# Performance work log

Measured on AMD Instinct MI355X. Metric: run time of the kernel, lower is better.

Reference implementation:

```python
import jax, jax.numpy as jnp
import numpy as np

NUM_HEADS = 16


def setup_inputs() -> dict:
    key = jax.random.key(0)
    ks = jax.random.split(key, 7)
    B, S, H = 4, 1024, 1024
    s = 0.02
    return {
        "x": jax.random.normal(ks[0], (B, S, H), dtype=jnp.float32),
        "Wq": jax.random.normal(ks[1], (H, H), dtype=jnp.float32) * s,
        "bq": jax.random.normal(ks[2], (H,), dtype=jnp.float32) * s,
        "Wk": jax.random.normal(ks[3], (H, H), dtype=jnp.float32) * s,
        "bk": jax.random.normal(ks[4], (H,), dtype=jnp.float32) * s,
        "Wv": jax.random.normal(ks[5], (H, H), dtype=jnp.float32) * s,
        "bv": jax.random.normal(ks[6], (H,), dtype=jnp.float32) * s,
    }


def _split_heads(y, num_heads):
    # rearrange 'b s (h c) -> h b s c'
    b, s, hid = y.shape
    c = hid // num_heads
    return y.reshape(b, s, num_heads, c).transpose(2, 0, 1, 3)


def reference(x, Wq, bq, Wk, bk, Wv, bv):
    h = NUM_HEADS
    head_size = x.shape[-1] // h
    # torch Linear: y = x @ W.T + b
    q = _split_heads(x @ Wq.T + bq, h)  # [h,b,s,c]
    k = _split_heads(x @ Wk.T + bk, h)
    v = _split_heads(x @ Wv.T + bv, h)
    scores = jnp.einsum('hbfc,hbtc->hbft', q, k) / jnp.sqrt(
        jnp.asarray(head_size, x.dtype))
    patterns = jax.nn.softmax(scores, axis=-1)  # softmax over t
    # NOTE: faithful to source, contracts over f (query axis) per
    # einsum('hbft,hbfc->hbtc', patterns, value)
    av = jnp.einsum('hbft,hbfc->hbtc', patterns, v)  # [h,b,t,c]
    # rearrange 'h b s c -> b s (c h)'  (channel-major interleave)
    out = av.transpose(1, 2, 3, 0)  # [b,s,c,h]
    b, s, c, hh = out.shape
    return out.reshape(b, s, c * hh)
```

## Files before the change

### kernel.cpp

```cpp
#include <hip/hip_runtime.h>
#include <hip/hip_bf16.h>

typedef short bf16x8 __attribute__((ext_vector_type(8)));
typedef short bf16x4 __attribute__((ext_vector_type(4)));
typedef float f32x4 __attribute__((ext_vector_type(4)));
typedef unsigned short u16;

#define MFMA32(a, b, c) __builtin_amdgcn_mfma_f32_16x16x32_bf16(a, b, c, 0, 0, 0)

#if defined(__has_builtin)
#if __has_builtin(__builtin_amdgcn_mfma_f32_16x16x16bf16_1k)
#define HAVE_MFMA16 1
#define MFMA16(a, b, c) __builtin_amdgcn_mfma_f32_16x16x16bf16_1k(a, b, c, 0, 0, 0)
#endif
#endif
#ifndef HAVE_MFMA16
static __device__ inline f32x4 mfma16_asm(bf16x4 a, bf16x4 b, f32x4 c) {
    f32x4 d;
    asm volatile("v_mfma_f32_16x16x16_bf16 %0, %1, %2, %3\n\ts_nop 7\n\ts_nop 7"
                 : "=v"(d) : "v"(a), "v"(b), "v"(c));
    return d;
}
#define MFMA16(a, b, c) mfma16_asm(a, b, c)
#endif

__device__ inline float fexp2(float x) {
#if defined(__has_builtin) && __has_builtin(__builtin_amdgcn_exp2f)
    return __builtin_amdgcn_exp2f(x);
#else
    return exp2f(x);
#endif
}

__device__ inline u16 f2bf(float f) {
    unsigned u = __float_as_uint(f);
    unsigned r = (u + 0x7fffu + ((u >> 16) & 1u)) >> 16;
    return (u16)r;
}

__device__ inline float bf2f(u16 v) {
    return __uint_as_float(((unsigned)v) << 16);
}

__device__ inline void gload_lds16(const void* g, void* l) {
    __builtin_amdgcn_global_load_lds(
        (const __attribute__((address_space(1))) void*)g,
        (__attribute__((address_space(3))) void*)l, 16, 0, 0);
}

#define BARRIER() __builtin_amdgcn_s_barrier()

__device__ inline int swz(int row, int colbyte) {
    return row * 128 + (colbyte ^ ((row & 7) << 4));
}

__device__ inline void stage8k_512(const u16* __restrict__ g, int gstride,
                                   u16* lds, int tid) {
    int o = tid * 16;
    int row = o >> 7;
    int colb = (o & 127) ^ ((row & 7) << 4);
    gload_lds16(g + row * gstride + (colb >> 1), (char*)lds + o);
}

__device__ inline void stage16k_256(const u16* __restrict__ g, int gstride,
                                    u16* lds, int tid) {
#pragma unroll
    for (int j = 0; j < 4; j++) {
        int o = (tid + j * 256) * 16;
        int row = o >> 7;
        int colb = (o & 127) ^ ((row & 7) << 4);
        gload_lds16(g + row * gstride + (colb >> 1), (char*)lds + o);
    }
}

__device__ inline void stage8k_256(const u16* __restrict__ g, int gstride,
                                   u16* lds, int tid) {
#pragma unroll
    for (int j = 0; j < 2; j++) {
        int o = (tid + j * 256) * 16;
        int row = o >> 7;
        int colb = (o & 127) ^ ((row & 7) << 4);
        gload_lds16(g + row * gstride + (colb >> 1), (char*)lds + o);
    }
}

__global__ void k_convert_all(const float* __restrict__ x,
                              const float* __restrict__ w0, const float* __restrict__ w1,
                              const float* __restrict__ w2,
                              u16* __restrict__ xb, u16* __restrict__ wb) {
    const int bid = blockIdx.x;
    const float* s;
    u16* d;
    int i;
    if (bid < 4096) {
        s = x; d = xb;
        i = bid * 1024 + threadIdx.x * 4;
    } else {
        int wsec = (bid - 4096) >> 10;
        int boff = (bid - 4096) & 1023;
        s = (wsec == 0) ? w0 : ((wsec == 1) ? w1 : w2);
        d = wb + wsec * 1048576;
        i = boff * 1024 + threadIdx.x * 4;
    }
    float4 v = *reinterpret_cast<const float4*>(s + i);
    ushort4 o;
    o.x = f2bf(v.x); o.y = f2bf(v.y); o.z = f2bf(v.z); o.w = f2bf(v.w);
    *reinterpret_cast<ushort4*>(d + i) = o;
}

__global__ __launch_bounds__(256, 6) void k_proj(
    const u16* __restrict__ xb, const u16* __restrict__ wb,
    const float* __restrict__ bq, const float* __restrict__ bk, const float* __restrict__ bv,
    u16* __restrict__ outQ, u16* __restrict__ outK, u16* __restrict__ outVt)
{
    __shared__ __align__(16) u16 As[8192];
    __shared__ __align__(16) u16 Bs[4096];
    const int tid = threadIdx.x;
    const int lane = tid & 63;
    const int w = tid >> 6;
    const int bid = blockIdx.x;
    const int xcd = bid & 7, idx = bid >> 3;
    const int mg = xcd & 3, ng = xcd >> 2;
    const int m0 = (mg * 8 + (idx & 7)) * 128;
    const int nfull = ng * 24 + (idx >> 3);
    const int widx = nfull >> 4;
    const int n0 = (nfull & 15) * 64;
    const u16* W = wb + widx * 1024 * 1024;
    const float* bias = (widx == 0) ? bq : ((widx == 1) ? bk : bv);

    const int wm = (w >> 1) * 64, wn = (w & 1) * 32;
    const int lm = lane & 15, lg = lane >> 4;

    f32x4 zero = {0.f, 0.f, 0.f, 0.f};
    f32x4 acc[4][2];
#pragma unroll
    for (int m = 0; m < 4; m++)
#pragma unroll
        for (int n = 0; n < 2; n++) acc[m][n] = zero;

    for (int it = 0; it < 16; ++it) {
        stage16k_256(xb + m0 * 1024 + it * 64, 1024, As, tid);
        stage8k_256(W + n0 * 1024 + it * 64, 1024, Bs, tid);
        __syncthreads();
        const char* Ab = (const char*)As;
        const char* Bb = (const char*)Bs;
#pragma unroll
        for (int kk = 0; kk < 2; kk++) {
            bf16x8 a[4], b[2];
#pragma unroll
            for (int m = 0; m < 4; m++)
                a[m] = *(const bf16x8*)(Ab + swz(wm + m * 16 + lm, kk * 64 + lg * 16));
#pragma unroll
            for (int n = 0; n < 2; n++)
                b[n] = *(const bf16x8*)(Bb + swz(wn + n * 16 + lm, kk * 64 + lg * 16));
#pragma unroll
            for (int m = 0; m < 4; m++)
#pragma unroll
                for (int n = 0; n < 2; n++)
                    acc[m][n] = MFMA32(a[m], b[n], acc[m][n]);
        }
        __syncthreads();
    }

#pragma unroll
    for (int n = 0; n < 2; n++) {
        int col = n0 + wn + n * 16 + lm;
        float bz = bias[col];
        int h = col >> 6, c = col & 63;
#pragma unroll
        for (int m = 0; m < 4; m++) {
#pragma unroll
            for (int r = 0; r < 4; r++) {
                int row = m0 + wm + m * 16 + lg * 4 + r;
                float v = acc[m][n][r] + bz;
                int bb = row >> 10, s = row & 1023;
                int hb = h * 4 + bb;
                if (widx == 0) {
                    outQ[(hb * 1024 + s) * 64 + c] = f2bf(v * 0.18033688011112042f);
                } else if (widx == 1) {
                    outK[(hb * 1024 + s) * 64 + c] = f2bf(v);
                } else {
                    outVt[(hb * 64 + c) * 1024 + s] = f2bf(v);
                }
            }
        }
    }
}

__global__ __launch_bounds__(512, 2) void k_stats(
    const u16* __restrict__ Q, const u16* __restrict__ K, float* __restrict__ linv_out)
{
    __shared__ __align__(16) u16 sK[2][4096];
    const int bid = blockIdx.x;
    const int hb = (bid & 7) * 8 + ((bid >> 3) & 7);
    const int fb = (bid >> 6) * 256;
    const int tid = threadIdx.x, lane = tid & 63, w = tid >> 6;
    const int lm = lane & 15, lg = lane >> 4;
    const u16* Qh = Q + hb * 65536;
    const u16* Kh = K + hb * 65536;

    bf16x8 a[2][2];
#pragma unroll
    for (int fg = 0; fg < 2; fg++) {
        const u16* qp = &Qh[(fb + w * 32 + fg * 16 + lm) * 64 + lg * 8];
        a[fg][0] = *(const bf16x8*)qp;
        a[fg][1] = *(const bf16x8*)(qp + 32);
    }

    float lrun[2][4] = {{0.f, 0.f, 0.f, 0.f}, {0.f, 0.f, 0.f, 0.f}};

    stage8k_512(Kh, 64, sK[0], tid);
    int cur = 0;
    for (int it = 0; it < 16; ++it) {
        if (it < 15) {
            stage8k_512(Kh + (it + 1) * 64 * 64, 64, sK[cur ^ 1], tid);
            asm volatile("s_waitcnt vmcnt(1)" ::: "memory");
        } else {
            asm volatile("s_waitcnt vmcnt(0)" ::: "memory");
        }
        BARRIER();
        const char* base = (const char*)sK[cur];
#pragma unroll
        for (int n = 0; n < 4; n++) {
            int r = n * 16 + lm;
            bf16x8 b0 = *(const bf16x8*)(base + swz(r, lg * 16));
            bf16x8 b1 = *(const bf16x8*)(base + swz(r, 64 + lg * 16));
#pragma unroll
            for (int fg = 0; fg < 2; fg++) {
                f32x4 z = {0.f, 0.f, 0.f, 0.f};
                z = MFMA32(a[fg][0], b0, z);
                z = MFMA32(a[fg][1], b1, z);
                lrun[fg][0] += fexp2(z[0]);
                lrun[fg][1] += fexp2(z[1]);
                lrun[fg][2] += fexp2(z[2]);
                lrun[fg][3] += fexp2(z[3]);
            }
        }
        BARRIER();
        cur ^= 1;
    }
#pragma unroll
    for (int fg = 0; fg < 2; fg++) {
#pragma unroll
        for (int r = 0; r < 4; r++) {
            float s = lrun[fg][r];
            s += __shfl_xor(s, 1);
            s += __shfl_xor(s, 2);
            s += __shfl_xor(s, 4);
            s += __shfl_xor(s, 8);
            if (lm == 0)
                linv_out[hb * 1024 + fb + w * 32 + fg * 16 + lg * 4 + r] = 1.0f / s;
        }
    }
}

__global__ __launch_bounds__(512, 2) void k_av(
    const u16* __restrict__ Q, const u16* __restrict__ K, const u16* __restrict__ Vt,
    const float* __restrict__ linv, u16* __restrict__ av_sb)
{
    __shared__ __align__(16) u16 sQ[2][4096];
    __shared__ __align__(16) u16 sV[2][4096];
    __shared__ __align__(16) float linv_lds[1024];
    const int bid = blockIdx.x;
    const int hb = (bid & 7) * 8 + ((bid >> 3) & 7);
    const int tb = (bid >> 6) * 256;
    const int tid = threadIdx.x, lane = tid & 63, w = tid >> 6;
    const int lm = lane & 15, lg = lane >> 4;
    const u16* Qh = Q + hb * 65536;
    const u16* Kh = K + hb * 65536;
    const u16* Vh = Vt + hb * 65536;
    const float* lh = linv + hb * 1024;

    bf16x8 bK[2][2];
#pragma unroll
    for (int tg = 0; tg < 2; tg++) {
        const u16* kp = &Kh[(tb + w * 32 + tg * 16 + lm) * 64 + lg * 8];
        bK[tg][0] = *(const bf16x8*)kp;
        bK[tg][1] = *(const bf16x8*)(kp + 32);
    }

    f32x4 zero = {0.f, 0.f, 0.f, 0.f};
    f32x4 accv[2][4];
#pragma unroll
    for (int tg = 0; tg < 2; tg++)
#pragma unroll
        for (int m = 0; m < 4; m++) accv[tg][m] = zero;

    stage8k_512(Qh, 64, sQ[0], tid);
    stage8k_512(Vh, 1024, sV[0], tid);
    *reinterpret_cast<float2*>(&linv_lds[tid * 2]) =
        *reinterpret_cast<const float2*>(&lh[tid * 2]);
    __syncthreads();

    int cur = 0;
    for (int it = 0; it < 16; ++it) {
        if (it < 15) {
            int fn = (it + 1) * 64;
            stage8k_512(Qh + fn * 64, 64, sQ[cur ^ 1], tid);
            stage8k_512(Vh + fn, 1024, sV[cur ^ 1], tid);
            asm volatile("s_waitcnt vmcnt(2)" ::: "memory");
        } else {
            asm volatile("s_waitcnt vmcnt(0)" ::: "memory");
        }
        if (it > 0) BARRIER();
        const char* Qb = (const char*)sQ[cur];
        const char* Vb = (const char*)sV[cur];
        const int fc = it * 64;

        bf16x4 afrag[2][4];
#pragma unroll
        for (int mq = 0; mq < 4; mq++) {
            bf16x8 aq0 = *(const bf16x8*)(Qb + swz(mq * 16 + lm, lg * 16));
            bf16x8 aq1 = *(const bf16x8*)(Qb + swz(mq * 16 + lm, 64 + lg * 16));
            float4 lv = *reinterpret_cast<const float4*>(&linv_lds[fc + mq * 16 + lg * 4]);
#pragma unroll
            for (int tg = 0; tg < 2; tg++) {
                f32x4 z = {0.f, 0.f, 0.f, 0.f};
                z = MFMA32(aq0, bK[tg][0], z);
                z = MFMA32(aq1, bK[tg][1], z);
                union { __hip_bfloat162 h2[2]; bf16x4 v4; } u;
                u.h2[0] = __float22bfloat162_rn(
                    make_float2(fexp2(z[0]) * lv.x, fexp2(z[1]) * lv.y));
                u.h2[1] = __float22bfloat162_rn(
                    make_float2(fexp2(z[2]) * lv.z, fexp2(z[3]) * lv.w));
                afrag[tg][mq] = u.v4;
            }
        }
        __builtin_amdgcn_s_setprio(1);
#pragma unroll
        for (int m = 0; m < 4; m++) {
#pragma unroll
            for (int kc = 0; kc < 4; kc++) {
                bf16x4 bv = *(const bf16x4*)(Vb + swz(m * 16 + lm, kc * 32 + lg * 8));
#pragma unroll
                for (int tg = 0; tg < 2; tg++)
                    accv[tg][m] = MFMA16(afrag[tg][kc], bv, accv[tg][m]);
            }
        }
        __builtin_amdgcn_s_setprio(0);
        BARRIER();
        cur ^= 1;
    }

    const int h = hb >> 2, bb = hb & 3;
#pragma unroll
    for (int tg = 0; tg < 2; tg++) {
#pragma unroll
        for (int m = 0; m < 4; m++) {
#pragma unroll
            for (int r = 0; r < 4; r++) {
                int t = tb + w * 32 + tg * 16 + lg * 4 + r;
                av_sb[((bb * 1024 + t) * 16 + h) * 64 + m * 16 + lm] = f2bf(accv[tg][m][r]);
            }
        }
    }
}

__global__ __launch_bounds__(256) void k_interleave(
    const u16* __restrict__ av_sb, float* __restrict__ out)
{
    const int bid = blockIdx.x;
    const int bb = bid >> 7, ts = (bid & 127) * 8;
    const int c = threadIdx.x & 63, tl = threadIdx.x >> 6;
#pragma unroll
    for (int p = 0; p < 2; p++) {
        int t = ts + p * 4 + tl;
        const u16* src = &av_sb[(bb * 1024 + t) * 1024];
        float4 w[4];
#pragma unroll
        for (int q = 0; q < 4; q++) {
#pragma unroll
            for (int j = 0; j < 4; j++) {
                int h = q * 4 + j;
                ((float*)&w[q])[j] = bf2f(src[h * 64 + c]);
            }
        }
        float4* dst = (float4*)&out[(bb * 1024 + t) * 1024 + c * 16];
        dst[0] = w[0]; dst[1] = w[1]; dst[2] = w[2]; dst[3] = w[3];
    }
}

extern "C" void kernel_launch(void* const* d_in, const int* in_sizes, int n_in,
                              void* d_out, int out_size, void* d_ws, size_t ws_size,
                              hipStream_t stream) {
    const float* x  = (const float*)d_in[0];
    const float* Wq = (const float*)d_in[1];
    const float* bq = (const float*)d_in[2];
    const float* Wk = (const float*)d_in[3];
    const float* bk = (const float*)d_in[4];
    const float* Wv = (const float*)d_in[5];
    const float* bv = (const float*)d_in[6];
    float* out = (float*)d_out;
    char* ws = (char*)d_ws;

    u16* xb = (u16*)ws;
    u16* wb = (u16*)(ws + (8u << 20));
    u16* Qb = (u16*)(ws + (14u << 20));
    u16* Kb = (u16*)(ws + (22u << 20));
    u16* Vt = (u16*)(ws + (30u << 20));
    float* linv = (float*)(ws + (38u << 20));
    u16* av_sb = (u16*)ws;

    k_convert_all<<<7168, 256, 0, stream>>>(x, Wq, Wk, Wv, xb, wb);
    k_proj<<<1536, 256, 0, stream>>>(xb, wb, bq, bk, bv, Qb, Kb, Vt);
    k_stats<<<256, 512, 0, stream>>>(Qb, Kb, linv);
    k_av<<<256, 512, 0, stream>>>(Qb, Kb, Vt, linv, av_sb);
    k_interleave<<<512, 256, 0, stream>>>(av_sb, out);
}
```

Before: 109.1 us.

## Shrink attention tiles to 64 rows per block and launch 4x more blocks

The stats and AV kernels now use 256-thread blocks that each handle 64 query/key rows instead of 512-thread blocks handling 256. The grid grows from 256 to 1024 blocks, so the 256 CUs of the MI355X can be better filled. In exchange, every block streams the full K (or Q and V^T) tiles from global memory for a quarter of the work, which quadruples redundant L2 traffic. Each wave also now handles one 16-row group instead of two, so there is less register reuse per staged LDS tile.

```diff
diff --git a/kernel.cpp b/kernel.cpp
--- a/kernel.cpp
+++ b/kernel.cpp
@@ -52,14 +52,6 @@
 
 __device__ inline int swz(int row, int colbyte) {
     return row * 128 + (colbyte ^ ((row & 7) << 4));
-}
-
-__device__ inline void stage8k_512(const u16* __restrict__ g, int gstride,
-                                   u16* lds, int tid) {
-    int o = tid * 16;
-    int row = o >> 7;
-    int colb = (o & 127) ^ ((row & 7) << 4);
-    gload_lds16(g + row * gstride + (colb >> 1), (char*)lds + o);
 }
 
 __device__ inline void stage16k_256(const u16* __restrict__ g, int gstride,
@@ -187,34 +179,30 @@
     }
 }
 
-__global__ __launch_bounds__(512, 2) void k_stats(
+__global__ __launch_bounds__(256, 4) void k_stats(
     const u16* __restrict__ Q, const u16* __restrict__ K, float* __restrict__ linv_out)
 {
     __shared__ __align__(16) u16 sK[2][4096];
     const int bid = blockIdx.x;
     const int hb = (bid & 7) * 8 + ((bid >> 3) & 7);
-    const int fb = (bid >> 6) * 256;
+    const int fb = (bid >> 6) * 64;
     const int tid = threadIdx.x, lane = tid & 63, w = tid >> 6;
     const int lm = lane & 15, lg = lane >> 4;
     const u16* Qh = Q + hb * 65536;
     const u16* Kh = K + hb * 65536;
 
-    bf16x8 a[2][2];
-#pragma unroll
-    for (int fg = 0; fg < 2; fg++) {
-        const u16* qp = &Qh[(fb + w * 32 + fg * 16 + lm) * 64 + lg * 8];
-        a[fg][0] = *(const bf16x8*)qp;
-        a[fg][1] = *(const bf16x8*)(qp + 32);
-    }
-
-    float lrun[2][4] = {{0.f, 0.f, 0.f, 0.f}, {0.f, 0.f, 0.f, 0.f}};
-
-    stage8k_512(Kh, 64, sK[0], tid);
+    const u16* qp = &Qh[(fb + w * 16 + lm) * 64 + lg * 8];
+    bf16x8 a0 = *(const bf16x8*)qp;
+    bf16x8 a1 = *(const bf16x8*)(qp + 32);
+
+    float lrun[4] = {0.f, 0.f, 0.f, 0.f};
+
+    stage8k_256(Kh, 64, sK[0], tid);
     int cur = 0;
     for (int it = 0; it < 16; ++it) {
         if (it < 15) {
-            stage8k_512(Kh + (it + 1) * 64 * 64, 64, sK[cur ^ 1], tid);
-            asm volatile("s_waitcnt vmcnt(1)" ::: "memory");
+            stage8k_256(Kh + (it + 1) * 4096, 64, sK[cur ^ 1], tid);
+            asm volatile("s_waitcnt vmcnt(2)" ::: "memory");
         } else {
             asm volatile("s_waitcnt vmcnt(0)" ::: "memory");
         }
@@ -225,36 +213,30 @@
             int r = n * 16 + lm;
             bf16x8 b0 = *(const bf16x8*)(base + swz(r, lg * 16));
             bf16x8 b1 = *(const bf16x8*)(base + swz(r, 64 + lg * 16));
-#pragma unroll
-            for (int fg = 0; fg < 2; fg++) {
-                f32x4 z = {0.f, 0.f, 0.f, 0.f};
-                z = MFMA32(a[fg][0], b0, z);
-                z = MFMA32(a[fg][1], b1, z);
-                lrun[fg][0] += fexp2(z[0]);
-                lrun[fg][1] += fexp2(z[1]);
-                lrun[fg][2] += fexp2(z[2]);
-                lrun[fg][3] += fexp2(z[3]);
-            }
+            f32x4 z = {0.f, 0.f, 0.f, 0.f};
+            z = MFMA32(a0, b0, z);
+            z = MFMA32(a1, b1, z);
+            lrun[0] += fexp2(z[0]);
+            lrun[1] += fexp2(z[1]);
+            lrun[2] += fexp2(z[2]);
+            lrun[3] += fexp2(z[3]);
         }
         BARRIER();
         cur ^= 1;
     }
 #pragma unroll
-    for (int fg = 0; fg < 2; fg++) {
-#pragma unroll
-        for (int r = 0; r < 4; r++) {
-            float s = lrun[fg][r];
-            s += __shfl_xor(s, 1);
-            s += __shfl_xor(s, 2);
-            s += __shfl_xor(s, 4);
-            s += __shfl_xor(s, 8);
-            if (lm == 0)
-                linv_out[hb * 1024 + fb + w * 32 + fg * 16 + lg * 4 + r] = 1.0f / s;
-        }
-    }
-}
-
-__global__ __launch_bounds__(512, 2) void k_av(
+    for (int r = 0; r < 4; r++) {
+        float s = lrun[r];
+        s += __shfl_xor(s, 1);
+        s += __shfl_xor(s, 2);
+        s += __shfl_xor(s, 4);
+        s += __shfl_xor(s, 8);
+        if (lm == 0)
+            linv_out[hb * 1024 + fb + w * 16 + lg * 4 + r] = 1.0f / s;
+    }
+}
+
+__global__ __launch_bounds__(256, 4) void k_av(
     const u16* __restrict__ Q, const u16* __restrict__ K, const u16* __restrict__ Vt,
     const float* __restrict__ linv, u16* __restrict__ av_sb)
 {
@@ -263,7 +245,7 @@
     __shared__ __align__(16) float linv_lds[1024];
     const int bid = blockIdx.x;
     const int hb = (bid & 7) * 8 + ((bid >> 3) & 7);
-    const int tb = (bid >> 6) * 256;
+    const int tb = (bid >> 6) * 64;
     const int tid = threadIdx.x, lane = tid & 63, w = tid >> 6;
     const int lm = lane & 15, lg = lane >> 4;
     const u16* Qh = Q + hb * 65536;
@@ -271,34 +253,28 @@
     const u16* Vh = Vt + hb * 65536;
     const float* lh = linv + hb * 1024;
 
-    bf16x8 bK[2][2];
-#pragma unroll
-    for (int tg = 0; tg < 2; tg++) {
-        const u16* kp = &Kh[(tb + w * 32 + tg * 16 + lm) * 64 + lg * 8];
-        bK[tg][0] = *(const bf16x8*)kp;
-        bK[tg][1] = *(const bf16x8*)(kp + 32);
-    }
+    const u16* kp = &Kh[(tb + w * 16 + lm) * 64 + lg * 8];
+    bf16x8 bK0 = *(const bf16x8*)kp;
+    bf16x8 bK1 = *(const bf16x8*)(kp + 32);
 
     f32x4 zero = {0.f, 0.f, 0.f, 0.f};
-    f32x4 accv[2][4];
-#pragma unroll
-    for (int tg = 0; tg < 2; tg++)
-#pragma unroll
-        for (int m = 0; m < 4; m++) accv[tg][m] = zero;
-
-    stage8k_512(Qh, 64, sQ[0], tid);
-    stage8k_512(Vh, 1024, sV[0], tid);
-    *reinterpret_cast<float2*>(&linv_lds[tid * 2]) =
-        *reinterpret_cast<const float2*>(&lh[tid * 2]);
+    f32x4 accv[4];
+#pragma unroll
+    for (int m = 0; m < 4; m++) accv[m] = zero;
+
+    stage8k_256(Qh, 64, sQ[0], tid);
+    stage8k_256(Vh, 1024, sV[0], tid);
+    *reinterpret_cast<float4*>(&linv_lds[tid * 4]) =
+        *reinterpret_cast<const float4*>(&lh[tid * 4]);
     __syncthreads();
 
     int cur = 0;
     for (int it = 0; it < 16; ++it) {
         if (it < 15) {
             int fn = (it + 1) * 64;
-            stage8k_512(Qh + fn * 64, 64, sQ[cur ^ 1], tid);
-            stage8k_512(Vh + fn, 1024, sV[cur ^ 1], tid);
-            asm volatile("s_waitcnt vmcnt(2)" ::: "memory");
+            stage8k_256(Qh + fn * 64, 64, sQ[cur ^ 1], tid);
+            stage8k_256(Vh + fn, 1024, sV[cur ^ 1], tid);
+            asm volatile("s_waitcnt vmcnt(4)" ::: "memory");
         } else {
             asm volatile("s_waitcnt vmcnt(0)" ::: "memory");
         }
@@ -307,24 +283,21 @@
         const char* Vb = (const char*)sV[cur];
         const int fc = it * 64;
 
-        bf16x4 afrag[2][4];
+        bf16x4 afrag[4];
 #pragma unroll
         for (int mq = 0; mq < 4; mq++) {
             bf16x8 aq0 = *(const bf16x8*)(Qb + swz(mq * 16 + lm, lg * 16));
             bf16x8 aq1 = *(const bf16x8*)(Qb + swz(mq * 16 + lm, 64 + lg * 16));
             float4 lv = *reinterpret_cast<const float4*>(&linv_lds[fc + mq * 16 + lg * 4]);
-#pragma unroll
-            for (int tg = 0; tg < 2; tg++) {
-                f32x4 z = {0.f, 0.f, 0.f, 0.f};
-                z = MFMA32(aq0, bK[tg][0], z);
-                z = MFMA32(aq1, bK[tg][1], z);
-                union { __hip_bfloat162 h2[2]; bf16x4 v4; } u;
-                u.h2[0] = __float22bfloat162_rn(
-                    make_float2(fexp2(z[0]) * lv.x, fexp2(z[1]) * lv.y));
-                u.h2[1] = __float22bfloat162_rn(
-                    make_float2(fexp2(z[2]) * lv.z, fexp2(z[3]) * lv.w));
-                afrag[tg][mq] = u.v4;
-            }
+            f32x4 z = {0.f, 0.f, 0.f, 0.f};
+            z = MFMA32(aq0, bK0, z);
+            z = MFMA32(aq1, bK1, z);
+            union { __hip_bfloat162 h2[2]; bf16x4 v4; } u;
+            u.h2[0] = __float22bfloat162_rn(
+                make_float2(fexp2(z[0]) * lv.x, fexp2(z[1]) * lv.y));
+            u.h2[1] = __float22bfloat162_rn(
+                make_float2(fexp2(z[2]) * lv.z, fexp2(z[3]) * lv.w));
+            afrag[mq] = u.v4;
         }
         __builtin_amdgcn_s_setprio(1);
 #pragma unroll
@@ -332,9 +305,7 @@
 #pragma unroll
             for (int kc = 0; kc < 4; kc++) {
                 bf16x4 bv = *(const bf16x4*)(Vb + swz(m * 16 + lm, kc * 32 + lg * 8));
-#pragma unroll
-                for (int tg = 0; tg < 2; tg++)
-                    accv[tg][m] = MFMA16(afrag[tg][kc], bv, accv[tg][m]);
+                accv[m] = MFMA16(afrag[kc], bv, accv[m]);
             }
         }
         __builtin_amdgcn_s_setprio(0);
@@ -344,14 +315,11 @@
 
     const int h = hb >> 2, bb = hb & 3;
 #pragma unroll
-    for (int tg = 0; tg < 2; tg++) {
-#pragma unroll
-        for (int m = 0; m < 4; m++) {
-#pragma unroll
-            for (int r = 0; r < 4; r++) {
-                int t = tb + w * 32 + tg * 16 + lg * 4 + r;
-                av_sb[((bb * 1024 + t) * 16 + h) * 64 + m * 16 + lm] = f2bf(accv[tg][m][r]);
-            }
+    for (int m = 0; m < 4; m++) {
+#pragma unroll
+        for (int r = 0; r < 4; r++) {
+            int t = tb + w * 16 + lg * 4 + r;
+            av_sb[((bb * 1024 + t) * 16 + h) * 64 + m * 16 + lm] = f2bf(accv[m][r]);
         }
     }
 }
@@ -403,7 +371,7 @@
 
     k_convert_all<<<7168, 256, 0, stream>>>(x, Wq, Wk, Wv, xb, wb);
     k_proj<<<1536, 256, 0, stream>>>(xb, wb, bq, bk, bv, Qb, Kb, Vt);
-    k_stats<<<256, 512, 0, stream>>>(Qb, Kb, linv);
-    k_av<<<256, 512, 0, stream>>>(Qb, Kb, Vt, linv, av_sb);
+    k_stats<<<1024, 256, 0, stream>>>(Qb, Kb, linv);
+    k_av<<<1024, 256, 0, stream>>>(Qb, Kb, Vt, linv, av_sb);
     k_interleave<<<512, 256, 0, stream>>>(av_sb, out);
 }
```

Result: slower. 151.0 us (+38.3%).

## Double-buffer projection GEMM and use one barrier per iteration in attention kernels

Applied to the files above, without the earlier changes.

The projection kernel gets double-buffered LDS tiles. The next K-slice is prefetched with global_load_lds while MFMAs run on the current slice, and setprio is raised around the MFMA block. The lrun and av kernels restructure their loops so each iteration waits on vmcnt(0) and takes a single barrier at the end instead of two. This is meant to hide global load latency and cut barrier overhead. The cost is twice the LDS in k_proj, with the occupancy hint dropped from 6 to 3 blocks.

```diff
diff --git a/kernel.cpp b/kernel.cpp
--- a/kernel.cpp
+++ b/kernel.cpp
@@ -49,6 +49,7 @@
 }
 
 #define BARRIER() __builtin_amdgcn_s_barrier()
+#define VMCNT0() asm volatile("s_waitcnt vmcnt(0)" ::: "memory")
 
 __device__ inline int swz(int row, int colbyte) {
     return row * 128 + (colbyte ^ ((row & 7) << 4));
@@ -108,13 +109,13 @@
     *reinterpret_cast<ushort4*>(d + i) = o;
 }
 
-__global__ __launch_bounds__(256, 6) void k_proj(
+__global__ __launch_bounds__(256, 3) void k_proj(
     const u16* __restrict__ xb, const u16* __restrict__ wb,
     const float* __restrict__ bq, const float* __restrict__ bk, const float* __restrict__ bv,
     u16* __restrict__ outQ, u16* __restrict__ outK, u16* __restrict__ outVt)
 {
-    __shared__ __align__(16) u16 As[8192];
-    __shared__ __align__(16) u16 Bs[4096];
+    __shared__ __align__(16) u16 As[2][8192];
+    __shared__ __align__(16) u16 Bs[2][4096];
     const int tid = threadIdx.x;
     const int lane = tid & 63;
     const int w = tid >> 6;
@@ -138,12 +139,19 @@
 #pragma unroll
         for (int n = 0; n < 2; n++) acc[m][n] = zero;
 
+    stage16k_256(xb + m0 * 1024, 1024, As[0], tid);
+    stage8k_256(W + n0 * 1024, 1024, Bs[0], tid);
+    VMCNT0();
+    BARRIER();
+
+    int cur = 0;
     for (int it = 0; it < 16; ++it) {
-        stage16k_256(xb + m0 * 1024 + it * 64, 1024, As, tid);
-        stage8k_256(W + n0 * 1024 + it * 64, 1024, Bs, tid);
-        __syncthreads();
-        const char* Ab = (const char*)As;
-        const char* Bb = (const char*)Bs;
+        if (it < 15) {
+            stage16k_256(xb + m0 * 1024 + (it + 1) * 64, 1024, As[cur ^ 1], tid);
+            stage8k_256(W + n0 * 1024 + (it + 1) * 64, 1024, Bs[cur ^ 1], tid);
+        }
+        const char* Ab = (const char*)As[cur];
+        const char* Bb = (const char*)Bs[cur];
 #pragma unroll
         for (int kk = 0; kk < 2; kk++) {
             bf16x8 a[4], b[2];
@@ -153,13 +161,19 @@
 #pragma unroll
             for (int n = 0; n < 2; n++)
                 b[n] = *(const bf16x8*)(Bb + swz(wn + n * 16 + lm, kk * 64 + lg * 16));
+            __builtin_amdgcn_s_setprio(1);
 #pragma unroll
             for (int m = 0; m < 4; m++)
 #pragma unroll
                 for (int n = 0; n < 2; n++)
                     acc[m][n] = MFMA32(a[m], b[n], acc[m][n]);
-        }
-        __syncthreads();
+            __builtin_amdgcn_s_setprio(0);
+        }
+        if (it < 15) {
+            VMCNT0();
+            BARRIER();
+        }
+        cur ^= 1;
     }
 
 #pragma unroll
@@ -210,15 +224,13 @@
     float lrun[2][4] = {{0.f, 0.f, 0.f, 0.f}, {0.f, 0.f, 0.f, 0.f}};
 
     stage8k_512(Kh, 64, sK[0], tid);
+    VMCNT0();
+    BARRIER();
+
     int cur = 0;
     for (int it = 0; it < 16; ++it) {
-        if (it < 15) {
-            stage8k_512(Kh + (it + 1) * 64 * 64, 64, sK[cur ^ 1], tid);
-            asm volatile("s_waitcnt vmcnt(1)" ::: "memory");
-        } else {
-            asm volatile("s_waitcnt vmcnt(0)" ::: "memory");
-        }
-        BARRIER();
+        if (it < 15)
+            stage8k_512(Kh + (it + 1) * 4096, 64, sK[cur ^ 1], tid);
         const char* base = (const char*)sK[cur];
 #pragma unroll
         for (int n = 0; n < 4; n++) {
@@ -236,7 +248,10 @@
                 lrun[fg][3] += fexp2(z[3]);
             }
         }
-        BARRIER();
+        if (it < 15) {
+            VMCNT0();
+            BARRIER();
+        }
         cur ^= 1;
     }
 #pragma unroll
@@ -290,6 +305,7 @@
     stage8k_512(Vh, 1024, sV[0], tid);
     *reinterpret_cast<float2*>(&linv_lds[tid * 2]) =
         *reinterpret_cast<const float2*>(&lh[tid * 2]);
+    VMCNT0();
     __syncthreads();
 
     int cur = 0;
@@ -298,11 +314,7 @@
             int fn = (it + 1) * 64;
             stage8k_512(Qh + fn * 64, 64, sQ[cur ^ 1], tid);
             stage8k_512(Vh + fn, 1024, sV[cur ^ 1], tid);
-            asm volatile("s_waitcnt vmcnt(2)" ::: "memory");
-        } else {
-            asm volatile("s_waitcnt vmcnt(0)" ::: "memory");
-        }
-        if (it > 0) BARRIER();
+        }
         const char* Qb = (const char*)sQ[cur];
         const char* Vb = (const char*)sV[cur];
         const int fc = it * 64;
@@ -338,7 +350,10 @@
             }
         }
         __builtin_amdgcn_s_setprio(0);
-        BARRIER();
+        if (it < 15) {
+            VMCNT0();
+            BARRIER();
+        }
         cur ^= 1;
     }
 
```

Result: faster. 105.4 us (-3.5%).
